# Kernel optimization log

Measured on AMD Instinct MI355X. Metric: run time of the kernel, lower is better.

The kernel has to match this reference:

```python
import jax, jax.numpy as jnp
import numpy as np

SUPPORT = 10
NEIGHBOR_NUM = 20
DEGREE = 8
NEG_SLOPE = 0.2
EPS = 1e-12


def _norm(x, axis):
    n = jnp.linalg.norm(x, axis=axis, keepdims=True)
    return x / jnp.maximum(n, EPS)


def knn_index(v, k):
    # v: (b, n, 3) -> (b, n, k) indices of k nearest (self excluded)
    inner = jnp.einsum('bnd,bmd->bnm', v, v)
    quad = jnp.sum(v * v, axis=2)
    dist = quad[:, :, None] - 2.0 * inner + quad[:, None, :]
    _, idx = jax.lax.top_k(-dist, k + 1)  # smallest distances
    return idx[:, :, 1:]


def gather_nb(feat, idx):
    # feat (b,n,c), idx (b,n,k) -> (b,n,k,c)
    b = feat.shape[0]
    return feat[jnp.arange(b)[:, None, None], idx]


def nb_dir_norm(vertices, idx):
    nb = gather_nb(vertices, idx) - vertices[:, :, None, :]
    return _norm(nb, axis=-1)


def op3d(idx, vertices, directions, kernel_num):
    # Conv_surface: directions (3, support*kernel)
    ndn = nb_dir_norm(vertices, idx)                 # (b,n,k,3)
    sdn = _norm(directions, axis=0)
    theta = jax.nn.relu(jnp.einsum('bnkd,de->bnke', ndn, sdn))
    b, n, kk, _ = theta.shape
    theta = theta.reshape(b, n, kk, SUPPORT, kernel_num)
    return jnp.sum(jnp.max(theta, axis=2), axis=2)    # (b,n,kernel)


def opnd(idx, vertices, feat, w, bias, directions, out_ch):
    # Conv_layer: w (in,(s+1)*out), bias ((s+1)*out), directions (3, s*out)
    ndn = nb_dir_norm(vertices, idx)
    sdn = _norm(directions, axis=0)
    theta = jax.nn.relu(jnp.einsum('bnkd,de->bnke', ndn, sdn))  # (b,n,k,s*out)
    fo = feat @ w + bias                                        # (b,n,(s+1)*out)
    fc = fo[:, :, :out_ch]
    fs = gather_nb(fo[:, :, out_ch:], idx)                      # (b,n,k,s*out)
    b, n, kk, _ = theta.shape
    act = (theta * fs).reshape(b, n, kk, SUPPORT, out_ch)
    return fc + jnp.sum(jnp.max(act, axis=2), axis=2)


def tree_gcn(x, w_root, w_branch, w_l1, w_l2, bias, activation):
    # depth-0 upsampling TreeGCN: x (b,node,in) -> (b,node*DEGREE,out)
    b, node, in_f = x.shape
    root = x @ w_root                                           # (b,node,out)
    br = jax.nn.leaky_relu(jnp.einsum('bni,nij->bnj', x, w_branch), NEG_SLOPE)
    br = br.reshape(b, node * DEGREE, in_f)
    br = (br @ w_l1) @ w_l2                                     # (b,node*deg,out)
    out = jnp.repeat(root, DEGREE, axis=1) + br
    if activation:
        out = jax.nn.leaky_relu(out + jnp.tile(bias, (1, node, 1)), NEG_SLOPE)
    return out


def setup_inputs() -> dict:
    key = jax.random.key(0)
    ks = iter(jax.random.split(key, 32))
    r = lambda shape: (jax.random.normal(next(ks), shape, dtype=jnp.float32) * 0.1)
    inp = {
        'coase_points': jax.random.normal(next(ks), (2, 512, 3), dtype=jnp.float32),
        'd0': r((3, SUPPORT * 32)),
        'w1': r((32, (SUPPORT + 1) * 64)), 'b1': r(((SUPPORT + 1) * 64,)), 'dir1': r((3, SUPPORT * 64)),
        'd2': r((3, SUPPORT * 32)),
        'w3': r((32, (SUPPORT + 1) * 64)), 'b3': r(((SUPPORT + 1) * 64,)), 'dir3': r((3, SUPPORT * 64)),
        'w4': r((64, (SUPPORT + 1) * 64)), 'b4': r(((SUPPORT + 1) * 64,)), 'dir4': r((3, SUPPORT * 64)),
        'w5': r((64, (SUPPORT + 1) * 64)), 'b5': r(((SUPPORT + 1) * 64,)), 'dir5': r((3, SUPPORT * 64)),
        'root1': r((64, 3)), 'branch1': r((512, 64, DEGREE * 64)),
        'loop1a': r((64, 64 * SUPPORT)), 'loop1b': r((64 * SUPPORT, 3)), 'bias1': r((1, DEGREE, 3)),
        'root2': r((64, 3)), 'branch2': r((4096, 64, DEGREE * 64)),
        'loop2a': r((64, 64 * SUPPORT)), 'loop2b': r((64 * SUPPORT, 3)),
    }
    return inp


def reference(coase_points, d0, w1, b1, dir1, d2, w3, b3, dir3, w4, b4, dir4,
              w5, b5, dir5, root1, branch1, loop1a, loop1b, bias1,
              root2, branch2, loop2a, loop2b):
    idx = knn_index(coase_points, NEIGHBOR_NUM)
    fm0 = jax.nn.relu(op3d(idx, coase_points, d0, 32))  # dropout is identity in eval
    fm1 = jax.nn.relu(opnd(idx, coase_points, fm0, w1, b1, dir1, 64))
    pc1 = tree_gcn(fm1, root1, branch1, loop1a, loop1b, bias1, True)   # (b, 4096, 3)
    idx2 = knn_index(pc1, NEIGHBOR_NUM)
    fm2 = jax.nn.relu(op3d(idx2, pc1, d2, 32))
    fm3 = jax.nn.relu(opnd(idx2, pc1, fm2, w3, b3, dir3, 64))
    fm4 = jax.nn.relu(opnd(idx2, pc1, fm3, w4, b4, dir4, 64))
    fm5 = jax.nn.relu(opnd(idx2, pc1, fm4, w5, b5, dir5, 64))
    pc2 = tree_gcn(fm5, root2, branch2, loop2a, loop2b, None, False)   # (b, 32768, 3)
    return pc1, pc2
```

## Files before the change

kernel.cpp:

```cpp
#include <hip/hip_runtime.h>
#include <hip/hip_bf16.h>
#include <stdint.h>

#define SUPPORT 10
#define KNN 20
#define DEGREE 8

__global__ __launch_bounds__(256) void prep_kernel(
    const float* __restrict__ d0, const float* __restrict__ dir1,
    const float* __restrict__ d2, const float* __restrict__ dir3,
    const float* __restrict__ dir4, const float* __restrict__ dir5,
    float* __restrict__ sdn0, float* __restrict__ sdn1, float* __restrict__ sdn2,
    float* __restrict__ sdn3, float* __restrict__ sdn4, float* __restrict__ sdn5,
    const float* __restrict__ l1a, const float* __restrict__ l1b,
    const float* __restrict__ l2a, const float* __restrict__ l2b,
    float* __restrict__ wc1, float* __restrict__ wc2,
    const float* __restrict__ pts1,
    float* __restrict__ px1, float* __restrict__ py1, float* __restrict__ pz1) {
#pragma clang fp contract(off)
  if (blockIdx.x < 13) {
    int t = blockIdx.x * 256 + threadIdx.x;
    if (t >= 3200) return;
    const float* src; float* dst; int cols; int e;
    if (t < 320)       { src = d0;   dst = sdn0; cols = 320; e = t; }
    else if (t < 960)  { src = dir1; dst = sdn1; cols = 640; e = t - 320; }
    else if (t < 1280) { src = d2;   dst = sdn2; cols = 320; e = t - 960; }
    else if (t < 1920) { src = dir3; dst = sdn3; cols = 640; e = t - 1280; }
    else if (t < 2560) { src = dir4; dst = sdn4; cols = 640; e = t - 1920; }
    else               { src = dir5; dst = sdn5; cols = 640; e = t - 2560; }
    float a = src[e], b = src[cols + e], c = src[2 * cols + e];
    float nrm = sqrtf(a * a + b * b + c * c);
    nrm = fmaxf(nrm, 1e-12f);
    dst[e] = a / nrm; dst[cols + e] = b / nrm; dst[2 * cols + e] = c / nrm;
  } else if (blockIdx.x < 15) {
    int which = blockIdx.x - 13;
    int tt = threadIdx.x;
    if (tt >= 192) return;
    const float* A  = which ? l2a : l1a;
    const float* Bm = which ? l2b : l1b;
    float* out = which ? wc2 : wc1;
    int i = tt / 3, c = tt % 3;
    float s = 0.f;
    for (int k = 0; k < 640; ++k) s = fmaf(A[i * 640 + k], Bm[k * 3 + c], s);
    out[i * 3 + c] = s;
  } else {
    int t = (blockIdx.x - 15) * 256 + threadIdx.x;
    if (t >= 1024) return;
    px1[t] = pts1[t * 3];
    py1[t] = pts1[t * 3 + 1];
    pz1[t] = pts1[t * 3 + 2];
  }
}

__global__ __launch_bounds__(256) void soa2_kernel(const float* __restrict__ pc1,
                                                   float* __restrict__ px,
                                                   float* __restrict__ py,
                                                   float* __restrict__ pz) {
  int t = blockIdx.x * 256 + threadIdx.x;
  if (t >= 8192) return;
  px[t] = pc1[t * 3];
  py[t] = pc1[t * 3 + 1];
  pz[t] = pc1[t * 3 + 2];
}

template <int MPER, int WAVES>
__global__ __launch_bounds__(WAVES * 64) void knn_kernel(
    const float* __restrict__ px, const float* __restrict__ py,
    const float* __restrict__ pz, int N, int* __restrict__ idx_out) {
#pragma clang fp contract(off)
  extern __shared__ uint32_t kbuf[];
  int w = threadIdx.x >> 6, lane = threadIdx.x & 63;
  int g = blockIdx.x * WAVES + w;
  int b = g / N, n = g % N;
  volatile uint32_t* K = kbuf + (size_t)w * 64 * MPER;
  const float* PX = px + (size_t)b * N;
  const float* PY = py + (size_t)b * N;
  const float* PZ = pz + (size_t)b * N;

  float nx = PX[n], ny = PY[n], nz = PZ[n];
  float qn = nx * nx + ny * ny + nz * nz;

  unsigned long long mymin = ~0ull;
  for (int j = 0; j < MPER; ++j) {
    int m = j * 64 + lane;
    float mx = PX[m], my = PY[m], mz = PZ[m];
    float inner = nx * mx + ny * my + nz * mz;
    float qm = mx * mx + my * my + mz * mz;
    float d = (qn - 2.0f * inner) + qm;
    uint32_t u = __float_as_uint(d);
    u ^= (u & 0x80000000u) ? 0xFFFFFFFFu : 0x80000000u;
    K[lane * MPER + (j ^ (lane & (MPER - 1)))] = u;
    unsigned long long key = ((unsigned long long)u << 32) | (unsigned)m;
    mymin = key < mymin ? key : mymin;
  }
  for (int r = 0; r < 21; ++r) {
    unsigned long long best = mymin;
#pragma unroll
    for (int s = 1; s < 64; s <<= 1) {
      unsigned long long o = __shfl_xor(best, s, 64);
      best = o < best ? o : best;
    }
    unsigned m = (unsigned)best;
    if (r > 0 && lane == 0) idx_out[(size_t)g * KNN + (r - 1)] = (int)m;
    if (r == 20) break;
    int owner = m & 63, slot = m >> 6;
    if (lane == slot) K[owner * MPER + (slot ^ (owner & (MPER - 1)))] = 0xFFFFFFFFu;
    unsigned long long cand = ~0ull;
    if (lane < MPER) {
      uint32_t v = K[owner * MPER + (lane ^ (owner & (MPER - 1)))];
      cand = ((unsigned long long)v << 32) | (unsigned)(lane * 64 + owner);
    }
#pragma unroll
    for (int s = 1; s < 64; s <<= 1) {
      unsigned long long o = __shfl_xor(cand, s, 64);
      cand = o < cand ? o : cand;
    }
    if (lane == owner) mymin = cand;
  }
}

__global__ __launch_bounds__(256) void ndn_kernel(const float* __restrict__ pts,
                                                  const int* __restrict__ idx,
                                                  float* __restrict__ ndn, int N) {
#pragma clang fp contract(off)
  int t = blockIdx.x * 256 + threadIdx.x;
  int total = 2 * N * KNN;
  if (t >= total) return;
  int k = t % KNN, g = t / KNN;
  int b = g / N, n = g % N;
  int m = idx[(size_t)g * KNN + k];
  const float* pb = pts + (size_t)b * N * 3;
  float dx = pb[m * 3] - pb[n * 3];
  float dy = pb[m * 3 + 1] - pb[n * 3 + 1];
  float dz = pb[m * 3 + 2] - pb[n * 3 + 2];
  float nr = sqrtf(dx * dx + dy * dy + dz * dz);
  nr = fmaxf(nr, 1e-12f);
  ndn[(size_t)t * 3] = dx / nr; ndn[(size_t)t * 3 + 1] = dy / nr; ndn[(size_t)t * 3 + 2] = dz / nr;
}

__global__ __launch_bounds__(256) void op3d_kernel(const float* __restrict__ ndn,
                                                   const float* __restrict__ sdn,
                                                   float* __restrict__ out, int N) {
#pragma clang fp contract(off)
  int c = threadIdx.x & 31;
  int g = (blockIdx.x * 256 + threadIdx.x) >> 5;
  if (g >= 2 * N) return;
  const float* nd = ndn + (size_t)g * 60;
  float sv0[SUPPORT], sv1[SUPPORT], sv2[SUPPORT], mm[SUPPORT];
#pragma unroll
  for (int s = 0; s < SUPPORT; ++s) {
    sv0[s] = sdn[s * 32 + c];
    sv1[s] = sdn[320 + s * 32 + c];
    sv2[s] = sdn[640 + s * 32 + c];
    mm[s] = 0.f;
  }
  for (int k = 0; k < KNN; ++k) {
    float nx = nd[k * 3], ny = nd[k * 3 + 1], nz = nd[k * 3 + 2];
#pragma unroll
    for (int s = 0; s < SUPPORT; ++s) {
      float t = nx * sv0[s] + ny * sv1[s] + nz * sv2[s];
      mm[s] = fmaxf(mm[s], t);
    }
  }
  float acc = 0.f;
#pragma unroll
  for (int s = 0; s < SUPPORT; ++s) acc += mm[s];
  out[(size_t)g * 32 + c] = acc;
}

template <int K>
__global__ __launch_bounds__(256) void fo_kernel(const float* __restrict__ feat,
                                                 const float* __restrict__ wmat,
                                                 const float* __restrict__ bias,
                                                 float* __restrict__ fo, int N) {
  __shared__ float fL[8 * K];
  int t = threadIdx.x;
  int gbase = blockIdx.x * 8;
  for (int i = t; i < 8 * K; i += 256) fL[i] = feat[(size_t)gbase * K + i];
  __syncthreads();
  float a0[8], a1[8], a2[8];
#pragma unroll
  for (int gg = 0; gg < 8; ++gg) { a0[gg] = 0.f; a1[gg] = 0.f; a2[gg] = 0.f; }
  bool has3 = (t < 192);
  for (int i = 0; i < K; ++i) {
    float w0 = wmat[i * 704 + t];
    float w1 = wmat[i * 704 + t + 256];
    float w2 = has3 ? wmat[i * 704 + t + 512] : 0.f;
#pragma unroll
    for (int gg = 0; gg < 8; ++gg) {
      float f = fL[gg * K + i];
      a0[gg] = fmaf(f, w0, a0[gg]);
      a1[gg] = fmaf(f, w1, a1[gg]);
      a2[gg] = fmaf(f, w2, a2[gg]);
    }
  }
  float b0 = bias[t], b1 = bias[t + 256], b2 = has3 ? bias[t + 512] : 0.f;
#pragma unroll
  for (int gg = 0; gg < 8; ++gg) {
    size_t base = (size_t)(gbase + gg) * 704;
    fo[base + t] = a0[gg] + b0;
    fo[base + t + 256] = a1[gg] + b1;
    if (has3) fo[base + t + 512] = a2[gg] + b2;
  }
}

__global__ __launch_bounds__(256) void opnd_kernel(const float* __restrict__ ndn,
                                                   const int* __restrict__ idx,
                                                   const float* __restrict__ fo,
                                                   const float* __restrict__ sdn,
                                                   float* __restrict__ fm, int N) {
#pragma clang fp contract(off)
  __shared__ float ndL[4][64];
  __shared__ int offL[4][24];
  int w = threadIdx.x >> 6, lane = threadIdx.x & 63;
  int g = blockIdx.x * 4 + w;
  if (lane < 60) ndL[w][lane] = ndn[(size_t)g * 60 + lane];
  if (lane < KNN) offL[w][lane] = ((g / N) * N + idx[(size_t)g * KNN + lane]) * 704 + 64;
  __syncthreads();
  const float* ndw = ndL[w];
  const int* offw = offL[w];
  float sv0[SUPPORT], sv1[SUPPORT], sv2[SUPPORT], mm[SUPPORT];
#pragma unroll
  for (int s = 0; s < SUPPORT; ++s) {
    sv0[s] = sdn[s * 64 + lane];
    sv1[s] = sdn[640 + s * 64 + lane];
    sv2[s] = sdn[1280 + s * 64 + lane];
    mm[s] = -__builtin_inff();
  }
  for (int k = 0; k < KNN; ++k) {
    float nx = ndw[k * 3], ny = ndw[k * 3 + 1], nz = ndw[k * 3 + 2];
    int off = offw[k];
#pragma unroll
    for (int s = 0; s < SUPPORT; ++s) {
      float t = fmaxf(nx * sv0[s] + ny * sv1[s] + nz * sv2[s], 0.f);
      float f = fo[(size_t)off + s * 64 + lane];
      mm[s] = fmaxf(mm[s], t * f);
    }
  }
  float acc = 0.f;
#pragma unroll
  for (int s = 0; s < SUPPORT; ++s) acc += mm[s];
  float fc = fo[(size_t)g * 704 + lane];
  float v = fc + acc;
  fm[(size_t)g * 64 + lane] = fmaxf(v, 0.f);
}

__global__ __launch_bounds__(256) void tree_exact_kernel(
    const float* __restrict__ x, const float* __restrict__ wroot,
    const float* __restrict__ wb, const float* __restrict__ l1,
    const float* __restrict__ l2, const float* __restrict__ bias,
    float* __restrict__ out, int node) {
#pragma clang fp contract(off)
  __shared__ float xL[2][64];
  __shared__ float brL[2][512];
  __shared__ float tL[16][640];
  __shared__ float rootv[2][3];
  int n = blockIdx.x, t = threadIdx.x;
  if (t < 128) xL[t >> 6][t & 63] = x[(size_t)(t >> 6) * node * 64 + (size_t)n * 64 + (t & 63)];
  __syncthreads();
  {
    const float* wrow = wb + (size_t)n * 64 * 512;
    int j0 = 2 * t;
    float a00 = 0.f, a01 = 0.f, a10 = 0.f, a11 = 0.f;
    for (int i = 0; i < 64; ++i) {
      float w0 = wrow[(size_t)i * 512 + j0];
      float w1 = wrow[(size_t)i * 512 + j0 + 1];
      float f0 = xL[0][i], f1 = xL[1][i];
      a00 = a00 + f0 * w0; a01 = a01 + f0 * w1;
      a10 = a10 + f1 * w0; a11 = a11 + f1 * w1;
    }
    brL[0][j0]     = a00 >= 0.f ? a00 : 0.2f * a00;
    brL[0][j0 + 1] = a01 >= 0.f ? a01 : 0.2f * a01;
    brL[1][j0]     = a10 >= 0.f ? a10 : 0.2f * a10;
    brL[1][j0 + 1] = a11 >= 0.f ? a11 : 0.2f * a11;
  }
  if (t < 6) {
    int b = t / 3, c = t % 3;
    float r = 0.f;
    for (int i = 0; i < 64; ++i) r = fmaf(xL[b][i], wroot[i * 3 + c], r);
    rootv[b][c] = r;
  }
  __syncthreads();
#pragma unroll 4
  for (int u = 0; u < 40; ++u) {
    int e = u * 256 + t;
    int p = e / 640, j = e % 640;
    const float* brow = brL[p >> 3] + (p & 7) * 64;
    float acc = 0.f;
    for (int i = 0; i < 64; ++i)
      acc = fmaf(brow[i], l1[i * 640 + j], acc);
    tL[p][j] = acc;
  }
  __syncthreads();
  if (t < 48) {
    int p = t / 3, c = t % 3, b = p >> 3, d = p & 7;
    float s = 0.f;
    for (int j = 0; j < 640; ++j) s = fmaf(tL[p][j], l2[j * 3 + c], s);
    float v = rootv[b][c] + s;
    v = v + bias[d * 3 + c];
    v = v >= 0.f ? v : 0.2f * v;
    out[((size_t)b * node * DEGREE + (size_t)n * DEGREE + d) * 3 + c] = v;
  }
}

__global__ __launch_bounds__(256) void tree_kernel(const float* __restrict__ x,
                                                   const float* __restrict__ wroot,
                                                   const float* __restrict__ wb,
                                                   const float* __restrict__ wc,
                                                   float* __restrict__ out,
                                                   int node) {
  __shared__ float xL[2][64];
  __shared__ float brL[2][512];
  int n = blockIdx.x;
  int t = threadIdx.x;
  if (t < 128) xL[t >> 6][t & 63] = x[(size_t)(t >> 6) * node * 64 + (size_t)n * 64 + (t & 63)];
  __syncthreads();
  float a00 = 0.f, a01 = 0.f, a10 = 0.f, a11 = 0.f;
  const float* wrow = wb + (size_t)n * 64 * 512;
  int j0 = 2 * t;
  for (int i = 0; i < 64; ++i) {
    float2 wv = *(const float2*)(wrow + (size_t)i * 512 + j0);
    float f0 = xL[0][i], f1 = xL[1][i];
    a00 += f0 * wv.x; a01 += f0 * wv.y;
    a10 += f1 * wv.x; a11 += f1 * wv.y;
  }
  brL[0][j0]     = a00 >= 0.f ? a00 : 0.2f * a00;
  brL[0][j0 + 1] = a01 >= 0.f ? a01 : 0.2f * a01;
  brL[1][j0]     = a10 >= 0.f ? a10 : 0.2f * a10;
  brL[1][j0 + 1] = a11 >= 0.f ? a11 : 0.2f * a11;
  __syncthreads();
  if (t < 48) {
    int b = t / 24, rem = t % 24, d = rem / 3, c = rem % 3;
    float root = 0.f, brs = 0.f;
    for (int i = 0; i < 64; ++i) {
      root = fmaf(xL[b][i], wroot[i * 3 + c], root);
      brs  = fmaf(brL[b][d * 64 + i], wc[i * 3 + c], brs);
    }
    float v = root + brs;
    out[((size_t)b * node * DEGREE + (size_t)n * DEGREE + d) * 3 + c] = v;
  }
}

extern "C" void kernel_launch(void* const* d_in, const int* in_sizes, int n_in,
                              void* d_out, int out_size, void* d_ws, size_t ws_size,
                              hipStream_t stream) {
  const float* pts1    = (const float*)d_in[0];
  const float* d0      = (const float*)d_in[1];
  const float* w1      = (const float*)d_in[2];
  const float* b1      = (const float*)d_in[3];
  const float* dir1    = (const float*)d_in[4];
  const float* d2      = (const float*)d_in[5];
  const float* w3      = (const float*)d_in[6];
  const float* b3      = (const float*)d_in[7];
  const float* dir3    = (const float*)d_in[8];
  const float* w4      = (const float*)d_in[9];
  const float* b4      = (const float*)d_in[10];
  const float* dir4    = (const float*)d_in[11];
  const float* w5      = (const float*)d_in[12];
  const float* b5      = (const float*)d_in[13];
  const float* dir5    = (const float*)d_in[14];
  const float* root1   = (const float*)d_in[15];
  const float* branch1 = (const float*)d_in[16];
  const float* l1a     = (const float*)d_in[17];
  const float* l1b     = (const float*)d_in[18];
  const float* bias1   = (const float*)d_in[19];
  const float* root2   = (const float*)d_in[20];
  const float* branch2 = (const float*)d_in[21];
  const float* l2a     = (const float*)d_in[22];
  const float* l2b     = (const float*)d_in[23];

  float* ws = (float*)d_ws;
  size_t o = 0;
  float* sdn0 = ws + o; o += 960;
  float* sdn1 = ws + o; o += 1920;
  float* sdn2 = ws + o; o += 960;
  float* sdn3 = ws + o; o += 1920;
  float* sdn4 = ws + o; o += 1920;
  float* sdn5 = ws + o; o += 1920;
  float* wc1  = ws + o; o += 192;
  float* wc2  = ws + o; o += 192;
  float* px1  = ws + o; o += 1024;
  float* py1  = ws + o; o += 1024;
  float* pz1  = ws + o; o += 1024;
  float* px2  = ws + o; o += 8192;
  float* py2  = ws + o; o += 8192;
  float* pz2  = ws + o; o += 8192;
  int*   idxb = (int*)(ws + o); o += (size_t)2 * 4096 * KNN;
  float* ndnb = ws + o; o += (size_t)2 * 4096 * KNN * 3;
  float* fo   = ws + o; o += (size_t)2 * 4096 * 704;
  float* fmA  = ws + o; o += (size_t)2 * 4096 * 64;
  float* fmB  = ws + o; o += (size_t)2 * 4096 * 64;

  float* pc1 = (float*)d_out;
  float* pc2 = (float*)d_out + 2 * 4096 * 3;

  prep_kernel<<<19, 256, 0, stream>>>(d0, dir1, d2, dir3, dir4, dir5,
                                      sdn0, sdn1, sdn2, sdn3, sdn4, sdn5,
                                      l1a, l1b, l2a, l2b, wc1, wc2,
                                      pts1, px1, py1, pz1);

  knn_kernel<8, 4><<<2 * 512 / 4, 256, 4 * 64 * 8 * 4, stream>>>(px1, py1, pz1, 512, idxb);
  ndn_kernel<<<(2 * 512 * KNN + 255) / 256, 256, 0, stream>>>(pts1, idxb, ndnb, 512);
  op3d_kernel<<<2 * 512 * 32 / 256, 256, 0, stream>>>(ndnb, sdn0, fmA, 512);
  fo_kernel<32><<<2 * 512 / 8, 256, 0, stream>>>(fmA, w1, b1, fo, 512);
  opnd_kernel<<<2 * 512 / 4, 256, 0, stream>>>(ndnb, idxb, fo, sdn1, fmB, 512);
  tree_exact_kernel<<<512, 256, 0, stream>>>(fmB, root1, branch1, l1a, l1b,
                                             bias1, pc1, 512);

  soa2_kernel<<<32, 256, 0, stream>>>(pc1, px2, py2, pz2);
  knn_kernel<64, 2><<<2 * 4096 / 2, 128, 2 * 64 * 64 * 4, stream>>>(px2, py2, pz2, 4096, idxb);
  ndn_kernel<<<(2 * 4096 * KNN + 255) / 256, 256, 0, stream>>>(pc1, idxb, ndnb, 4096);
  op3d_kernel<<<2 * 4096 * 32 / 256, 256, 0, stream>>>(ndnb, sdn2, fmA, 4096);
  fo_kernel<32><<<2 * 4096 / 8, 256, 0, stream>>>(fmA, w3, b3, fo, 4096);
  opnd_kernel<<<2 * 4096 / 4, 256, 0, stream>>>(ndnb, idxb, fo, sdn3, fmB, 4096);
  fo_kernel<64><<<2 * 4096 / 8, 256, 0, stream>>>(fmB, w4, b4, fo, 4096);
  opnd_kernel<<<2 * 4096 / 4, 256, 0, stream>>>(ndnb, idxb, fo, sdn4, fmA, 4096);
  fo_kernel<64><<<2 * 4096 / 8, 256, 0, stream>>>(fmA, w5, b5, fo, 4096);
  opnd_kernel<<<2 * 4096 / 4, 256, 0, stream>>>(ndnb, idxb, fo, sdn5, fmB, 4096);
  tree_kernel<<<4096, 256, 0, stream>>>(fmB, root2, branch2, wc2, pc2, 4096);
}
```

Measured before the change: 671.0 us.

## Replace LDS-backed kNN selection with per-lane top-4 registers and recompute fallback

Result: slower. 783.0 us (+16.7%).

```diff
diff --git a/kernel.cpp b/kernel.cpp
--- a/kernel.cpp
+++ b/kernel.cpp
@@ -63,16 +63,28 @@
   pz[t] = pc1[t * 3 + 2];
 }
 
+__device__ __forceinline__ void ins4(unsigned long long key,
+                                     unsigned long long& t0, unsigned long long& t1,
+                                     unsigned long long& t2, unsigned long long& t3) {
+  if (key < t3) {
+    if (key < t2) {
+      t3 = t2;
+      if (key < t1) {
+        t2 = t1;
+        if (key < t0) { t1 = t0; t0 = key; } else { t1 = key; }
+      } else { t2 = key; }
+    } else { t3 = key; }
+  }
+}
+
 template <int MPER, int WAVES>
 __global__ __launch_bounds__(WAVES * 64) void knn_kernel(
     const float* __restrict__ px, const float* __restrict__ py,
     const float* __restrict__ pz, int N, int* __restrict__ idx_out) {
 #pragma clang fp contract(off)
-  extern __shared__ uint32_t kbuf[];
   int w = threadIdx.x >> 6, lane = threadIdx.x & 63;
   int g = blockIdx.x * WAVES + w;
   int b = g / N, n = g % N;
-  volatile uint32_t* K = kbuf + (size_t)w * 64 * MPER;
   const float* PX = px + (size_t)b * N;
   const float* PY = py + (size_t)b * N;
   const float* PZ = pz + (size_t)b * N;
@@ -80,7 +92,9 @@
   float nx = PX[n], ny = PY[n], nz = PZ[n];
   float qn = nx * nx + ny * ny + nz * nz;
 
-  unsigned long long mymin = ~0ull;
+  unsigned long long t0 = ~0ull, t1 = ~0ull, t2 = ~0ull, t3 = ~0ull;
+  unsigned long long popmask = 0ull;
+
   for (int j = 0; j < MPER; ++j) {
     int m = j * 64 + lane;
     float mx = PX[m], my = PY[m], mz = PZ[m];
@@ -89,12 +103,11 @@
     float d = (qn - 2.0f * inner) + qm;
     uint32_t u = __float_as_uint(d);
     u ^= (u & 0x80000000u) ? 0xFFFFFFFFu : 0x80000000u;
-    K[lane * MPER + (j ^ (lane & (MPER - 1)))] = u;
-    unsigned long long key = ((unsigned long long)u << 32) | (unsigned)m;
-    mymin = key < mymin ? key : mymin;
-  }
+    ins4(((unsigned long long)u << 32) | (unsigned)m, t0, t1, t2, t3);
+  }
+
   for (int r = 0; r < 21; ++r) {
-    unsigned long long best = mymin;
+    unsigned long long best = t0;
 #pragma unroll
     for (int s = 1; s < 64; s <<= 1) {
       unsigned long long o = __shfl_xor(best, s, 64);
@@ -103,19 +116,28 @@
     unsigned m = (unsigned)best;
     if (r > 0 && lane == 0) idx_out[(size_t)g * KNN + (r - 1)] = (int)m;
     if (r == 20) break;
-    int owner = m & 63, slot = m >> 6;
-    if (lane == slot) K[owner * MPER + (slot ^ (owner & (MPER - 1)))] = 0xFFFFFFFFu;
-    unsigned long long cand = ~0ull;
-    if (lane < MPER) {
-      uint32_t v = K[owner * MPER + (lane ^ (owner & (MPER - 1)))];
-      cand = ((unsigned long long)v << 32) | (unsigned)(lane * 64 + owner);
-    }
-#pragma unroll
-    for (int s = 1; s < 64; s <<= 1) {
-      unsigned long long o = __shfl_xor(cand, s, 64);
-      cand = o < cand ? o : cand;
-    }
-    if (lane == owner) mymin = cand;
+    int owner = m & 63, jwin = m >> 6;
+    if (lane == owner) {
+      popmask |= 1ull << jwin;
+      t0 = t1; t1 = t2; t2 = t3; t3 = ~0ull;
+    }
+    bool dry = (t0 == ~0ull) && (__builtin_popcountll(popmask) < MPER);
+    if (__any(dry)) {
+      if (dry) {
+        t1 = t2 = t3 = ~0ull;
+        for (int j = 0; j < MPER; ++j) {
+          if ((popmask >> j) & 1ull) continue;
+          int mm = j * 64 + lane;
+          float mx = PX[mm], my = PY[mm], mz = PZ[mm];
+          float inner = nx * mx + ny * my + nz * mz;
+          float qm = mx * mx + my * my + mz * mz;
+          float d = (qn - 2.0f * inner) + qm;
+          uint32_t u = __float_as_uint(d);
+          u ^= (u & 0x80000000u) ? 0xFFFFFFFFu : 0x80000000u;
+          ins4(((unsigned long long)u << 32) | (unsigned)mm, t0, t1, t2, t3);
+        }
+      }
+    }
   }
 }
 
@@ -212,8 +234,10 @@
 #pragma clang fp contract(off)
   __shared__ float ndL[4][64];
   __shared__ int offL[4][24];
+  int nb = gridDim.x;
+  int lb = (blockIdx.x & 7) * (nb >> 3) + (blockIdx.x >> 3);
   int w = threadIdx.x >> 6, lane = threadIdx.x & 63;
-  int g = blockIdx.x * 4 + w;
+  int g = lb * 4 + w;
   if (lane < 60) ndL[w][lane] = ndn[(size_t)g * 60 + lane];
   if (lane < KNN) offL[w][lane] = ((g / N) * N + idx[(size_t)g * KNN + lane]) * 704 + 64;
   __syncthreads();
@@ -399,7 +423,7 @@
                                       l1a, l1b, l2a, l2b, wc1, wc2,
                                       pts1, px1, py1, pz1);
 
-  knn_kernel<8, 4><<<2 * 512 / 4, 256, 4 * 64 * 8 * 4, stream>>>(px1, py1, pz1, 512, idxb);
+  knn_kernel<8, 4><<<2 * 512 / 4, 256, 0, stream>>>(px1, py1, pz1, 512, idxb);
   ndn_kernel<<<(2 * 512 * KNN + 255) / 256, 256, 0, stream>>>(pts1, idxb, ndnb, 512);
   op3d_kernel<<<2 * 512 * 32 / 256, 256, 0, stream>>>(ndnb, sdn0, fmA, 512);
   fo_kernel<32><<<2 * 512 / 8, 256, 0, stream>>>(fmA, w1, b1, fo, 512);
@@ -408,7 +432,7 @@
                                              bias1, pc1, 512);
 
   soa2_kernel<<<32, 256, 0, stream>>>(pc1, px2, py2, pz2);
-  knn_kernel<64, 2><<<2 * 4096 / 2, 128, 2 * 64 * 64 * 4, stream>>>(px2, py2, pz2, 4096, idxb);
+  knn_kernel<64, 4><<<2 * 4096 / 4, 256, 0, stream>>>(px2, py2, pz2, 4096, idxb);
   ndn_kernel<<<(2 * 4096 * KNN + 255) / 256, 256, 0, stream>>>(pc1, idxb, ndnb, 4096);
   op3d_kernel<<<2 * 4096 * 32 / 256, 256, 0, stream>>>(ndnb, sdn2, fmA, 4096);
   fo_kernel<32><<<2 * 4096 / 8, 256, 0, stream>>>(fmA, w3, b3, fo, 4096);
```
